# Optimization experiments

Hardware: AMD Instinct MI355X
Metric: run time of the kernel (lower is better)

The kernel has to match this reference:

```python
import jax, jax.numpy as jnp
import numpy as np

G = 50000            # number of 5-node crystal graphs
NPG = 5              # nodes per graph (forward reshapes to (-1, 5, F))
N = G * NPG          # total nodes
IN = 64              # in_size (61 atomic-number feats + 3 position)
OUT = 64             # out_size
HID = 2 * OUT        # hidden width per __init__


def setup_inputs() -> dict:
    key = jax.random.key(0)
    ks = jax.random.split(key, 8)
    h = jax.random.normal(ks[0], (N, IN - 3), jnp.float32)
    x = jax.random.normal(ks[1], (N, 3), jnp.float32)
    # complete graph with self-loops inside each 5-node crystal
    base = np.arange(G, dtype=np.int64) * NPG
    li = np.repeat(np.arange(NPG, dtype=np.int64), NPG)
    lj = np.tile(np.arange(NPG, dtype=np.int64), NPG)
    src = jnp.asarray((base[:, None] + li[None, :]).reshape(-1))
    dst = jnp.asarray((base[:, None] + lj[None, :]).reshape(-1))

    def lin(k, fi, fo):
        return jax.random.normal(k, (fi, fo), jnp.float32) / np.float32(np.sqrt(fi))

    W1 = lin(ks[2], IN, HID);  b1 = jnp.zeros((HID,), jnp.float32)
    W2 = lin(ks[3], HID, HID); b2 = jnp.zeros((HID,), jnp.float32)
    W3 = lin(ks[4], HID, HID); b3 = jnp.zeros((HID,), jnp.float32)
    W4 = lin(ks[5], HID, OUT); b4 = jnp.zeros((OUT,), jnp.float32)
    return {"h": h, "x": x, "src": src, "dst": dst,
            "W1": W1, "b1": b1, "W2": W2, "b2": b2,
            "W3": W3, "b3": b3, "W4": W4, "b4": b4}


def _graph_conv(feat, src, dst, W, b):
    # DGL GraphConv, norm='both': D_dst^{-1/2} A D_src^{-1/2} X W + b
    e = src.shape[0]
    ones = jnp.ones((e,), feat.dtype)
    deg_out = jax.ops.segment_sum(ones, src, num_segments=N)
    deg_in = jax.ops.segment_sum(ones, dst, num_segments=N)
    norm_src = jax.lax.rsqrt(jnp.maximum(deg_out, 1.0))
    norm_dst = jax.lax.rsqrt(jnp.maximum(deg_in, 1.0))
    norm_e = norm_src[src] * norm_dst[dst]                      # [E]
    agg = jax.ops.segment_sum(feat[src] * norm_e[:, None], dst,
                              num_segments=N)                   # [N, F]
    return agg @ W + b


def reference(h, x, src, dst, W1, b1, W2, b2, W3, b3, W4, b4):
    hx = jnp.concatenate([h, x.astype(jnp.float32)], axis=1)   # [N, IN]
    f1 = _graph_conv(hx, src, dst, W1, b1)
    f2 = _graph_conv(f1, src, dst, W2, b2)
    f3 = _graph_conv(f2, src, dst, W3, b3)
    f4 = _graph_conv(f3, src, dst, W4, b4)                      # [N, OUT]
    return jnp.mean(f4.reshape((-1, NPG, f4.shape[-1])), axis=1)  # [G, OUT]
```

## Files before the change

### kernel.cpp

```cpp
#include <hip/hip_runtime.h>


#define GB 16

__global__ void __launch_bounds__(256) collapse1(
    const float* __restrict__ W1, const float* __restrict__ b1,
    const float* __restrict__ W2, const float* __restrict__ b2,
    const float* __restrict__ W3, const float* __restrict__ b3,
    const float* __restrict__ W4, const float* __restrict__ b4,
    float* __restrict__ ws) {
  __shared__ __align__(16) float smem[128 * 128 + 512];
  int tid = threadIdx.x;
  int bx = blockIdx.x;

  if (bx < 32) {
    float* W2s = smem;
    float* w1s = smem + 16384;
    int i0 = bx * 2;
    {
      const float4* s = (const float4*)W2;
      float4* d = (float4*)W2s;
      #pragma unroll
      for (int j = 0; j < 16; ++j) d[tid + 256 * j] = s[tid + 256 * j];
      if (tid < 64) ((float4*)w1s)[tid] = ((const float4*)(W1 + i0 * 128))[tid];
    }
    __syncthreads();
    int il = tid >> 7, oo = tid & 127;
    float s0 = 0.f, s1 = 0.f, s2 = 0.f, s3 = 0.f;
    #pragma unroll 8
    for (int k = 0; k < 128; k += 4) {
      s0 += w1s[il * 128 + k + 0] * W2s[(k + 0) * 128 + oo];
      s1 += w1s[il * 128 + k + 1] * W2s[(k + 1) * 128 + oo];
      s2 += w1s[il * 128 + k + 2] * W2s[(k + 2) * 128 + oo];
      s3 += w1s[il * 128 + k + 3] * W2s[(k + 3) * 128 + oo];
    }
    ws[(i0 + il) * 128 + oo] = (s0 + s1) + (s2 + s3);
    if (bx == 0 && tid < 128) {
      float s = b2[tid];
      #pragma unroll 4
      for (int k = 0; k < 128; ++k) s += b1[k] * W2s[k * 128 + tid];
      ws[16384 + tid] = s;
    }
  } else {
    float* W4s = smem;
    float* w3s = smem + 8192;
    int i0 = (bx - 32) * 4;
    {
      const float4* s = (const float4*)W4;
      float4* d = (float4*)W4s;
      #pragma unroll
      for (int j = 0; j < 8; ++j) d[tid + 256 * j] = s[tid + 256 * j];
      if (tid < 128) ((float4*)w3s)[tid] = ((const float4*)(W3 + i0 * 128))[tid];
    }
    __syncthreads();
    int il = tid >> 6, o = tid & 63;
    float s0 = 0.f, s1 = 0.f, s2 = 0.f, s3 = 0.f;
    #pragma unroll 8
    for (int k = 0; k < 128; k += 4) {
      s0 += w3s[il * 128 + k + 0] * W4s[(k + 0) * 64 + o];
      s1 += w3s[il * 128 + k + 1] * W4s[(k + 1) * 64 + o];
      s2 += w3s[il * 128 + k + 2] * W4s[(k + 2) * 64 + o];
      s3 += w3s[il * 128 + k + 3] * W4s[(k + 3) * 64 + o];
    }
    ws[8192 + (i0 + il) * 64 + o] = (s0 + s1) + (s2 + s3);
    if (bx == 32 && tid < 64) {
      float s = b4[tid];
      #pragma unroll 4
      for (int k = 0; k < 128; ++k) s += b3[k] * W4s[k * 64 + tid];
      ws[16512 + tid] = s;
    }
  }
}

__global__ void __launch_bounds__(256) collapse2(float* __restrict__ ws) {
  __shared__ __align__(16) float smem[128 * 64 + 512];
  float* Bms = smem;
  float* As  = smem + 8192;
  int tid = threadIdx.x;
  int i0 = blockIdx.x * 4;
  {
    const float4* s = (const float4*)(ws + 8192);
    float4* d = (float4*)Bms;
    #pragma unroll
    for (int j = 0; j < 8; ++j) d[tid + 256 * j] = s[tid + 256 * j];
    if (tid < 128) ((float4*)As)[tid] = ((const float4*)(ws + i0 * 128))[tid];
  }
  __syncthreads();
  int il = tid >> 6, o = tid & 63;
  float s0 = 0.f, s1 = 0.f, s2 = 0.f, s3 = 0.f;
  #pragma unroll 8
  for (int k = 0; k < 128; k += 4) {
    s0 += As[il * 128 + k + 0] * Bms[(k + 0) * 64 + o];
    s1 += As[il * 128 + k + 1] * Bms[(k + 1) * 64 + o];
    s2 += As[il * 128 + k + 2] * Bms[(k + 2) * 64 + o];
    s3 += As[il * 128 + k + 3] * Bms[(k + 3) * 64 + o];
  }
  ws[16640 + (i0 >> 2) * 256 + o * 4 + il] = ((s0 + s1) + (s2 + s3)) * 0.2f;
  if (blockIdx.x == 0 && tid < 64) {
    float s = ws[16512 + tid];
    #pragma unroll 4
    for (int k = 0; k < 128; ++k) s += ws[16384 + k] * Bms[k * 64 + tid];
    ws[20736 + tid] = s;
  }
}

__global__ void __launch_bounds__(256) gcn_main(
    const float* __restrict__ h, const float* __restrict__ x,
    const float* __restrict__ ws, float* __restrict__ out, int G) {
  __shared__ __align__(16) float hs[GB * 305];
  __shared__ __align__(16) float xs[GB * 15 + 4];
  __shared__ __align__(16) float m_s[GB][64];

  int tid = threadIdx.x;
  long gbase = (long)blockIdx.x * GB;
  if (gbase >= G) return;
  int ng = (int)min((long)GB, (long)(G - gbase));
  int o = tid & 63;

  float bco = ws[20736 + o];

  if (ng == GB) {
    const float4* hsrc = (const float4*)(h + gbase * 305);
    const float4* xsrc = (const float4*)(x + gbase * 15);
    float4* hdst = (float4*)hs;
    float4* xdst = (float4*)xs;
    #pragma unroll
    for (int r = 0; r < 5; ++r) {
      int i = tid + 256 * r;
      if (i < GB * 305 / 4) hdst[i] = hsrc[i];
    }
    if (tid < GB * 15 / 4) xdst[tid] = xsrc[tid];
  } else {
    for (int i = tid; i < ng * 305; i += 256) hs[i] = h[gbase * 305 + i];
    for (int i = tid; i < ng * 15; i += 256) xs[i] = x[gbase * 15 + i];
  }
  __syncthreads();

  int wv = tid >> 6, lane = tid & 63;

  #pragma unroll
  for (int j = 0; j < 4; ++j) {
    int g = wv * 4 + j;
    float a;
    if (lane < 61) {
      const float* hb = hs + g * 305 + lane;
      a = hb[0] + hb[61] + hb[122] + hb[183] + hb[244];
    } else {
      const float* xb = xs + g * 15 + (lane - 61);
      a = xb[0] + xb[3] + xb[6] + xb[9] + xb[12];
    }
    m_s[g][lane] = a;
  }

  {
    const float4* Wg = (const float4*)(ws + 16640);
    const float4* m0 = (const float4*)&m_s[wv * 4 + 0][0];
    const float4* m1 = (const float4*)&m_s[wv * 4 + 1][0];
    const float4* m2 = (const float4*)&m_s[wv * 4 + 2][0];
    const float4* m3 = (const float4*)&m_s[wv * 4 + 3][0];
    float a0 = bco, a1 = bco, a2 = bco, a3 = bco;
    #pragma unroll 4
    for (int q = 0; q < 16; ++q) {
      float4 w = Wg[q * 64 + o];
      float4 v0 = m0[q];
      float4 v1 = m1[q];
      float4 v2 = m2[q];
      float4 v3 = m3[q];
      a0 += v0.x * w.x + v0.y * w.y + v0.z * w.z + v0.w * w.w;
      a1 += v1.x * w.x + v1.y * w.y + v1.z * w.z + v1.w * w.w;
      a2 += v2.x * w.x + v2.y * w.y + v2.z * w.z + v2.w * w.w;
      a3 += v3.x * w.x + v3.y * w.y + v3.z * w.z + v3.w * w.w;
    }
    long ob = (gbase + wv * 4) * 64 + o;
    int gl = wv * 4;
    if (gl + 0 < ng) out[ob + 0]   = a0;
    if (gl + 1 < ng) out[ob + 64]  = a1;
    if (gl + 2 < ng) out[ob + 128] = a2;
    if (gl + 3 < ng) out[ob + 192] = a3;
  }
}

extern "C" void kernel_launch(void* const* d_in, const int* in_sizes, int n_in,
                              void* d_out, int out_size, void* d_ws, size_t ws_size,
                              hipStream_t stream) {
  const float* h  = (const float*)d_in[0];
  const float* x  = (const float*)d_in[1];
  const float* W1 = (const float*)d_in[4];
  const float* b1 = (const float*)d_in[5];
  const float* W2 = (const float*)d_in[6];
  const float* b2 = (const float*)d_in[7];
  const float* W3 = (const float*)d_in[8];
  const float* b3 = (const float*)d_in[9];
  const float* W4 = (const float*)d_in[10];
  const float* b4 = (const float*)d_in[11];
  float* ws = (float*)d_ws;
  float* out = (float*)d_out;

  int G = in_sizes[0] / 305;

  collapse1<<<64, 256, 0, stream>>>(W1, b1, W2, b2, W3, b3, W4, b4, ws);
  collapse2<<<16, 256, 0, stream>>>(ws);

  int blocks = (G + GB - 1) / GB;
  gcn_main<<<blocks, 256, 0, stream>>>(h, x, ws, out, G);
}
```

Before: 38.85 us.

## Process 64 graphs per block with lane-per-graph GEMV and scalar weight loads

Each block now handles 64 graphs, staging node features in four rounds of 16 into shared memory and storing the per-graph node sums transposed (feature-major, padded). In the output GEMV each lane owns one graph and each wavefront owns 16 output columns. The collapsed weight matrix is read with wave-uniform addresses, which allows scalar loads, and results are written as float4 rows. This cuts the per-graph weight reloads and the global weight traffic, and the weight layout written by collapse2 is changed to match. The cost is four times fewer blocks, extra barriers between rounds, and 16 accumulators per thread.

```diff
diff --git a/kernel.cpp b/kernel.cpp
--- a/kernel.cpp
+++ b/kernel.cpp
@@ -1,7 +1,8 @@
 #include <hip/hip_runtime.h>
 
 
-#define GB 16
+#define GB 64
+#define RG 16
 
 __global__ void __launch_bounds__(256) collapse1(
     const float* __restrict__ W1, const float* __restrict__ b1,
@@ -95,7 +96,7 @@
     s2 += As[il * 128 + k + 2] * Bms[(k + 2) * 64 + o];
     s3 += As[il * 128 + k + 3] * Bms[(k + 3) * 64 + o];
   }
-  ws[16640 + (i0 >> 2) * 256 + o * 4 + il] = ((s0 + s1) + (s2 + s3)) * 0.2f;
+  ws[16640 + (i0 + il) * 64 + o] = ((s0 + s1) + (s2 + s3)) * 0.2f;
   if (blockIdx.x == 0 && tid < 64) {
     float s = ws[16512 + tid];
     #pragma unroll 4
@@ -107,76 +108,83 @@
 __global__ void __launch_bounds__(256) gcn_main(
     const float* __restrict__ h, const float* __restrict__ x,
     const float* __restrict__ ws, float* __restrict__ out, int G) {
-  __shared__ __align__(16) float hs[GB * 305];
-  __shared__ __align__(16) float xs[GB * 15 + 4];
-  __shared__ __align__(16) float m_s[GB][64];
+  __shared__ __align__(16) float hs[RG * 305];
+  __shared__ __align__(16) float xs[RG * 15];
+  __shared__ __align__(16) float m_s[64][65];
 
   int tid = threadIdx.x;
   long gbase = (long)blockIdx.x * GB;
   if (gbase >= G) return;
   int ng = (int)min((long)GB, (long)(G - gbase));
-  int o = tid & 63;
-
-  float bco = ws[20736 + o];
-
-  if (ng == GB) {
-    const float4* hsrc = (const float4*)(h + gbase * 305);
-    const float4* xsrc = (const float4*)(x + gbase * 15);
-    float4* hdst = (float4*)hs;
-    float4* xdst = (float4*)xs;
+  int wv = tid >> 6, lane = tid & 63;
+  int nrounds = (ng + RG - 1) / RG;
+
+  for (int r = 0; r < nrounds; ++r) {
+    if (r > 0) __syncthreads();
+    int ngr = min(RG, ng - r * RG);
+    long gr = gbase + r * RG;
+    {
+      const float4* hsrc = (const float4*)(h + gr * 305);
+      float4* hdst = (float4*)hs;
+      int nh4 = (ngr * 305) >> 2;
+      #pragma unroll
+      for (int p = 0; p < 5; ++p) {
+        int i = tid + 256 * p;
+        if (i < nh4) hdst[i] = hsrc[i];
+      }
+      int hrem = ngr * 305 - nh4 * 4;
+      if (tid < hrem) hs[nh4 * 4 + tid] = h[gr * 305 + nh4 * 4 + tid];
+      const float4* xsrc = (const float4*)(x + gr * 15);
+      float4* xdst = (float4*)xs;
+      int nx4 = (ngr * 15) >> 2;
+      if (tid < nx4) xdst[tid] = xsrc[tid];
+      int xrem = ngr * 15 - nx4 * 4;
+      if (tid >= 64 && tid < 64 + xrem)
+        xs[nx4 * 4 + (tid - 64)] = x[gr * 15 + nx4 * 4 + (tid - 64)];
+    }
+    __syncthreads();
     #pragma unroll
-    for (int r = 0; r < 5; ++r) {
-      int i = tid + 256 * r;
-      if (i < GB * 305 / 4) hdst[i] = hsrc[i];
-    }
-    if (tid < GB * 15 / 4) xdst[tid] = xsrc[tid];
-  } else {
-    for (int i = tid; i < ng * 305; i += 256) hs[i] = h[gbase * 305 + i];
-    for (int i = tid; i < ng * 15; i += 256) xs[i] = x[gbase * 15 + i];
+    for (int j = 0; j < 4; ++j) {
+      int gl = wv * 4 + j;
+      if (gl < ngr) {
+        int gblk = r * RG + gl;
+        float a;
+        if (lane < 61) {
+          const float* hb = hs + gl * 305 + lane;
+          a = hb[0] + hb[61] + hb[122] + hb[183] + hb[244];
+        } else {
+          const float* xb = xs + gl * 15 + (lane - 61);
+          a = xb[0] + xb[3] + xb[6] + xb[9] + xb[12];
+        }
+        m_s[lane][gblk] = a;
+      }
+    }
   }
   __syncthreads();
 
-  int wv = tid >> 6, lane = tid & 63;
-
-  #pragma unroll
-  for (int j = 0; j < 4; ++j) {
-    int g = wv * 4 + j;
-    float a;
-    if (lane < 61) {
-      const float* hb = hs + g * 305 + lane;
-      a = hb[0] + hb[61] + hb[122] + hb[183] + hb[244];
-    } else {
-      const float* xb = xs + g * 15 + (lane - 61);
-      a = xb[0] + xb[3] + xb[6] + xb[9] + xb[12];
-    }
-    m_s[g][lane] = a;
-  }
-
   {
-    const float4* Wg = (const float4*)(ws + 16640);
-    const float4* m0 = (const float4*)&m_s[wv * 4 + 0][0];
-    const float4* m1 = (const float4*)&m_s[wv * 4 + 1][0];
-    const float4* m2 = (const float4*)&m_s[wv * 4 + 2][0];
-    const float4* m3 = (const float4*)&m_s[wv * 4 + 3][0];
-    float a0 = bco, a1 = bco, a2 = bco, a3 = bco;
-    #pragma unroll 4
-    for (int q = 0; q < 16; ++q) {
-      float4 w = Wg[q * 64 + o];
-      float4 v0 = m0[q];
-      float4 v1 = m1[q];
-      float4 v2 = m2[q];
-      float4 v3 = m3[q];
-      a0 += v0.x * w.x + v0.y * w.y + v0.z * w.z + v0.w * w.w;
-      a1 += v1.x * w.x + v1.y * w.y + v1.z * w.z + v1.w * w.w;
-      a2 += v2.x * w.x + v2.y * w.y + v2.z * w.z + v2.w * w.w;
-      a3 += v3.x * w.x + v3.y * w.y + v3.z * w.z + v3.w * w.w;
-    }
-    long ob = (gbase + wv * 4) * 64 + o;
-    int gl = wv * 4;
-    if (gl + 0 < ng) out[ob + 0]   = a0;
-    if (gl + 1 < ng) out[ob + 64]  = a1;
-    if (gl + 2 < ng) out[ob + 128] = a2;
-    if (gl + 3 < ng) out[ob + 192] = a3;
+    int obase = __builtin_amdgcn_readfirstlane(wv << 4);
+    const float* __restrict__ Wr = ws + 16640 + obase;
+    const float* __restrict__ bcp = ws + 20736 + obase;
+    float acc[16];
+    #pragma unroll
+    for (int j = 0; j < 16; ++j) acc[j] = bcp[j];
+
+    #pragma unroll 2
+    for (int k = 0; k < 64; ++k) {
+      float mk = m_s[k][lane];
+      const float* wk = Wr + k * 64;
+      #pragma unroll
+      for (int j = 0; j < 16; ++j) acc[j] += mk * wk[j];
+    }
+
+    if (lane < ng) {
+      float4* op = (float4*)(out + (gbase + lane) * 64 + obase);
+      op[0] = make_float4(acc[0],  acc[1],  acc[2],  acc[3]);
+      op[1] = make_float4(acc[4],  acc[5],  acc[6],  acc[7]);
+      op[2] = make_float4(acc[8],  acc[9],  acc[10], acc[11]);
+      op[3] = make_float4(acc[12], acc[13], acc[14], acc[15]);
+    }
   }
 }
 
```

Result: slower. 44.15 us (+13.6%).
